# Kernel tuning notes

Hardware: AMD Instinct MI355X
Metric: run time of the kernel (lower is better)

Reference implementation:

```python
import jax, jax.numpy as jnp
import numpy as np

D_INPUT = 1024
N_HEADS = 16
D_INNER = 64
SEQ = 1024
PREV = 1024
BS = 4
LN_EPS = 1e-5


def _rel_shift(x):
    # x: (i, j, b, h) -> Transformer-XL relative shift trick
    i, j, b, h = x.shape
    zero_pad = jnp.zeros((i, 1, b, h), dtype=x.dtype)
    return jnp.concatenate([zero_pad, x], axis=1).reshape(j + 1, i, b, h)[1:].reshape(i, j, b, h)


def setup_inputs() -> dict:
    key = jax.random.key(0)
    ks = jax.random.split(key, 9)
    w = 0.02
    return {
        "input_": jax.random.normal(ks[0], (SEQ, BS, D_INPUT), jnp.float32),
        "pos_embs": jax.random.normal(ks[1], (SEQ + PREV, D_INPUT), jnp.float32),
        "memory": jax.random.normal(ks[2], (PREV, BS, D_INPUT), jnp.float32),
        "u": jax.random.normal(ks[3], (N_HEADS, D_INNER), jnp.float32) * w,
        "v": jax.random.normal(ks[4], (N_HEADS, D_INNER), jnp.float32) * w,
        "W_kv": jax.random.normal(ks[5], (D_INPUT, 2 * N_HEADS * D_INNER), jnp.float32) * w,
        "W_q": jax.random.normal(ks[6], (D_INPUT, N_HEADS * D_INNER), jnp.float32) * w,
        "W_p": jax.random.normal(ks[7], (D_INPUT, N_HEADS * D_INNER), jnp.float32) * w,
        "W_out": jax.random.normal(ks[8], (N_HEADS * D_INNER, D_INPUT), jnp.float32) * w,
        "ln_g": jnp.ones((D_INPUT,), jnp.float32),
        "ln_b": jnp.zeros((D_INPUT,), jnp.float32),
    }


def reference(input_, pos_embs, memory, u, v, W_kv, W_q, W_p, W_out, ln_g, ln_b):
    S, B, D = input_.shape
    P = memory.shape[0]
    T = S + P
    H, d = u.shape
    scale = 1.0 / (d ** 0.5)

    x_mem = jnp.concatenate([memory, input_], axis=0)          # (T, B, D)
    kv = x_mem @ W_kv                                          # (T, B, 2*H*d)
    k, val = jnp.split(kv, 2, axis=-1)
    k = k.reshape(T, B, H, d)
    val = val.reshape(T, B, H, d)
    q = (input_ @ W_q).reshape(S, B, H, d)                     # (S, B, H, d)

    content_attn = jnp.einsum('ibhd,jbhd->ijbh', q + u, k)     # (S, T, B, H)
    p = (pos_embs @ W_p).reshape(T, H, d)                      # (T, H, d)
    position_attn = jnp.einsum('ibhd,jhd->ijbh', q + v, p)     # (S, T, B, H)
    position_attn = _rel_shift(position_attn)

    attn = jax.nn.softmax((content_attn + position_attn) * scale, axis=1)
    awv = jnp.einsum('ijbh,jbhd->ibhd', attn, val).reshape(S, B, H * d)

    out = input_ + awv @ W_out                                 # residual
    mu = jnp.mean(out, axis=-1, keepdims=True)
    var = jnp.mean(jnp.square(out - mu), axis=-1, keepdims=True)
    return (out - mu) * jax.lax.rsqrt(var + LN_EPS) * ln_g + ln_b
```

## Files before the change

### kernel.cpp

```cpp
#include <hip/hip_runtime.h>
#include <cstdint>
#include <cstddef>

#define S_  1024
#define B_  4
#define T_  2048
#define H_  16

typedef short     short8 __attribute__((ext_vector_type(8)));
typedef float     f32x4  __attribute__((ext_vector_type(4)));
typedef unsigned short u16x8 __attribute__((ext_vector_type(8)));

__device__ __forceinline__ unsigned short f2b(float f){
  uint32_t x = __builtin_bit_cast(uint32_t, f);
  x = (x + 0x7fffu + ((x >> 16) & 1u)) >> 16;
  return (unsigned short)x;
}
__device__ __forceinline__ unsigned short f2bt(float f){
  return (unsigned short)(__builtin_bit_cast(uint32_t, f) >> 16);
}
__device__ __forceinline__ float b2f(unsigned short u){
  return __builtin_bit_cast(float, ((uint32_t)u) << 16);
}

__device__ __forceinline__ void gl_lds16(const unsigned short* g, unsigned short* l){
  __builtin_amdgcn_global_load_lds(
      (const __attribute__((address_space(1))) void*)g,
      (__attribute__((address_space(3))) void*)l,
      16, 0, 0);
}

__global__ __launch_bounds__(256) void cvt_cat(
    const float* __restrict__ a, const float* __restrict__ bsrc,
    int splitElems, int total, unsigned short* __restrict__ out)
{
  int i = (blockIdx.x * 256 + threadIdx.x) * 4;
  if (i >= total) return;
  const float* src = (i < splitElems) ? (a + i) : (bsrc + (i - splitElems));
  float4 x = *(const float4*)src;
  ushort4 o;
  o.x = f2b(x.x); o.y = f2b(x.y); o.z = f2b(x.z); o.w = f2b(x.w);
  *(ushort4*)(out + i) = o;
}

__global__ __launch_bounds__(256) void wtrans(
    const float* __restrict__ in, unsigned short* __restrict__ out, int R, int C)
{
  __shared__ float tile[32][33];
  const int R0 = blockIdx.y * 32, C0 = blockIdx.x * 32;
  const int t = threadIdx.x;
  const int r = t >> 3, c4 = (t & 7) * 4;
  float4 x = *(const float4*)(in + (size_t)(R0 + r) * C + C0 + c4);
  tile[r][c4+0] = x.x; tile[r][c4+1] = x.y; tile[r][c4+2] = x.z; tile[r][c4+3] = x.w;
  __syncthreads();
  ushort4 o;
  o.x = f2b(tile[c4+0][r]); o.y = f2b(tile[c4+1][r]);
  o.z = f2b(tile[c4+2][r]); o.w = f2b(tile[c4+3][r]);
  *(ushort4*)(out + (size_t)(C0 + r) * R + R0 + c4) = o;
}

__global__ __launch_bounds__(256) void vtrans(
    const unsigned short* __restrict__ kvb, unsigned short* __restrict__ vtg)
{
  __shared__ __align__(16) unsigned short tile[64][72];
  const int t = threadIdx.x;
  const int bh = blockIdx.y;
  const int b = bh >> 4, h = bh & 15;
  const int t0 = blockIdx.x * 64;
  #pragma unroll
  for (int l = 0; l < 2; ++l){
    int idx = t + l * 256;
    int row = idx >> 3, seg = (idx & 7) * 8;
    u16x8 x = *(const u16x8*)(kvb + ((size_t)(t0 + row) * 4 + b) * 2048 + 1024 + h * 64 + seg);
    *(u16x8*)&tile[row][seg] = x;
  }
  __syncthreads();
  #pragma unroll
  for (int l = 0; l < 2; ++l){
    int idx = t + l * 256;
    int d = idx >> 3, nseg = (idx & 7) * 8;
    u16x8 o;
    #pragma unroll
    for (int j = 0; j < 8; ++j) o[j] = tile[nseg + j][d];
    *(u16x8*)(vtg + ((size_t)bh * 64 + d) * 2048 + t0 + nseg) = o;
  }
}

#define AS_IDX(row,k) ((((row) >> 3) * 512) + (((k) >> 3) * 64) + (((row) & 7) * 8) + ((k) & 7))

__global__ __launch_bounds__(256) void gemm_multi(
    const unsigned short* __restrict__ xb,
    const unsigned short* __restrict__ posb,
    const unsigned short* __restrict__ WkvT,
    const unsigned short* __restrict__ WqT,
    const unsigned short* __restrict__ WpT,
    unsigned short* __restrict__ kvb,
    unsigned short* __restrict__ qbb,
    unsigned short* __restrict__ pbb)
{
  const unsigned short *A, *BT;
  unsigned short* C;
  int N, local;
  int bx = blockIdx.x;
  if (bx < 1024){       A = xb;                       BT = WkvT; C = kvb; N = 2048; local = bx;        }
  else if (bx < 1280){  A = xb + (size_t)4096 * 1024; BT = WqT;  C = qbb; N = 1024; local = bx - 1024; }
  else {                A = posb;                     BT = WpT;  C = pbb; N = 1024; local = bx - 1280; }
  const int nb = N >> 7;
  const int M0 = (local / nb) * 128, N0 = (local % nb) * 128;
  const int K = 1024;

  __shared__ __align__(16) unsigned short As[128 * 64];
  __shared__ __align__(16) unsigned short Bs[128 * 64];
  const int t = threadIdx.x;
  const int w = t >> 6, lane = t & 63, quad = lane >> 4, l16 = lane & 15;
  const int wm = (w >> 1) * 64, wn = (w & 1) * 64;
  const int lr = lane & 7, lcb = lane >> 3;

  f32x4 acc[4][4] = {};

  for (int k0 = 0; k0 < K; k0 += 64){
    __syncthreads();
    #pragma unroll
    for (int i = 0; i < 4; ++i){
      int blk = 4 * w + i;
      gl_lds16(A  + (size_t)(M0 + 8 * blk + lr) * K + k0 + lcb * 8, As + blk * 512);
      gl_lds16(BT + (size_t)(N0 + 8 * blk + lr) * K + k0 + lcb * 8, Bs + blk * 512);
    }
    __syncthreads();
    #pragma unroll
    for (int ks = 0; ks < 2; ++ks){
      short8 af[4], bf[4];
      #pragma unroll
      for (int rt = 0; rt < 4; ++rt)
        af[rt] = *(short8*)&As[AS_IDX(wm + rt * 16 + l16, ks * 32 + quad * 8)];
      #pragma unroll
      for (int ct = 0; ct < 4; ++ct)
        bf[ct] = *(short8*)&Bs[AS_IDX(wn + ct * 16 + l16, ks * 32 + quad * 8)];
      #pragma unroll
      for (int rt = 0; rt < 4; ++rt)
        #pragma unroll
        for (int ct = 0; ct < 4; ++ct)
          acc[rt][ct] = __builtin_amdgcn_mfma_f32_16x16x32_bf16(af[rt], bf[ct], acc[rt][ct], 0, 0, 0);
    }
  }

  #pragma unroll
  for (int rt = 0; rt < 4; ++rt)
    #pragma unroll
    for (int r = 0; r < 4; ++r){
      int row = M0 + wm + rt * 16 + quad * 4 + r;
      #pragma unroll
      for (int ct = 0; ct < 4; ++ct)
        C[(size_t)row * N + N0 + wn + ct * 16 + l16] = f2b(acc[rt][ct][r]);
    }
}

__global__ __launch_bounds__(256) void gemm_outk(
    const unsigned short* __restrict__ A,
    const unsigned short* __restrict__ BT,
    float* __restrict__ OutP)
{
  const int K = 1024, N = 1024;
  const int k0s = blockIdx.z * 512, k0e = k0s + 512;
  float* outF = OutP + (size_t)blockIdx.z * 4096 * 1024;

  __shared__ __align__(16) unsigned short As[128 * 64];
  __shared__ __align__(16) unsigned short Bs[128 * 64];
  const int t = threadIdx.x;
  const int M0 = blockIdx.y * 128, N0 = blockIdx.x * 128;
  const int w = t >> 6, lane = t & 63, quad = lane >> 4, l16 = lane & 15;
  const int wm = (w >> 1) * 64, wn = (w & 1) * 64;
  const int lr = lane & 7, lcb = lane >> 3;

  f32x4 acc[4][4] = {};

  for (int k0 = k0s; k0 < k0e; k0 += 64){
    __syncthreads();
    #pragma unroll
    for (int i = 0; i < 4; ++i){
      int blk = 4 * w + i;
      gl_lds16(A  + (size_t)(M0 + 8 * blk + lr) * K + k0 + lcb * 8, As + blk * 512);
      gl_lds16(BT + (size_t)(N0 + 8 * blk + lr) * K + k0 + lcb * 8, Bs + blk * 512);
    }
    __syncthreads();
    #pragma unroll
    for (int ks = 0; ks < 2; ++ks){
      short8 af[4], bf[4];
      #pragma unroll
      for (int rt = 0; rt < 4; ++rt)
        af[rt] = *(short8*)&As[AS_IDX(wm + rt * 16 + l16, ks * 32 + quad * 8)];
      #pragma unroll
      for (int ct = 0; ct < 4; ++ct)
        bf[ct] = *(short8*)&Bs[AS_IDX(wn + ct * 16 + l16, ks * 32 + quad * 8)];
      #pragma unroll
      for (int rt = 0; rt < 4; ++rt)
        #pragma unroll
        for (int ct = 0; ct < 4; ++ct)
          acc[rt][ct] = __builtin_amdgcn_mfma_f32_16x16x32_bf16(af[rt], bf[ct], acc[rt][ct], 0, 0, 0);
    }
  }

  #pragma unroll
  for (int rt = 0; rt < 4; ++rt)
    #pragma unroll
    for (int r = 0; r < 4; ++r){
      int row = M0 + wm + rt * 16 + quad * 4 + r;
      #pragma unroll
      for (int ct = 0; ct < 4; ++ct)
        outF[(size_t)row * N + N0 + wn + ct * 16 + l16] = acc[rt][ct][r];
    }
}

__global__ __launch_bounds__(256, 3) void attn_mfma(
    const unsigned short* __restrict__ qb,
    const unsigned short* __restrict__ kvb,
    const unsigned short* __restrict__ pbm,
    const unsigned short* __restrict__ vtg,
    const float* __restrict__ ub, const float* __restrict__ vb,
    unsigned short* __restrict__ opart,
    float* __restrict__ lpart)
{
  __shared__ __align__(16) unsigned short Kc[64 * 64];
  __shared__ __align__(16) unsigned short VT[64 * 64];
  __shared__ __align__(16) unsigned short Pw[128 * 64];
  __shared__ __align__(16) unsigned short Pb[64 * 72];
  __shared__ unsigned short Sc[64 * 65];

  const int t = threadIdx.x;
  const int i0 = blockIdx.x * 64;
  const int bh = blockIdx.y;
  const int jh = blockIdx.z;
  const int b = bh >> 4, h = bh & 15;
  const int w = t >> 6, lane = t & 63, quad = lane >> 4, l16 = lane & 15;
  const int colbase = h * 64 + quad * 8;
  const int ctLo = 3 - w;

  short8 qu[2], qv[2][2];
  #pragma unroll
  for (int cs = 0; cs < 2; ++cs){
    int gr = i0 + 16 * w + l16 + cs;
    #pragma unroll
    for (int ks = 0; ks < 2; ++ks){
      u16x8 q8 = *(const u16x8*)(qb + ((size_t)gr * 4 + b) * 1024 + colbase + ks * 32);
      #pragma unroll
      for (int j = 0; j < 8; ++j){
        float f = b2f(q8[j]);
        qv[cs][ks][j] = (short)f2b(f + vb[colbase + ks * 32 + j]);
        if (cs == 0) qu[ks][j] = (short)f2b(f + ub[colbase + ks * 32 + j]);
      }
    }
  }

  f32x4 oacc[4] = {};
  float lsum[4] = {0.f, 0.f, 0.f, 0.f};

  u16x8 pk[2], pv2[2], pp[4];

  auto loadRegs = [&](int jc){
    const int j0 = jc * 64;
    const int D = j0 - i0;
    #pragma unroll
    for (int l = 0; l < 2; ++l){
      int idx = t + l * 256;
      int row = idx >> 3, cb = idx & 7;
      pk[l]  = *(const u16x8*)(kvb + ((size_t)(j0 + row) * 4 + b) * 2048 + h * 64 + cb * 8);
      pv2[l] = *(const u16x8*)(vtg + ((size_t)bh * 64 + row) * 2048 + j0 + cb * 8);
    }
    #pragma unroll
    for (int l = 0; l < 4; ++l){
      int idx = t + l * 256;
      int row = idx >> 3, cb = idx & 7;
      int pr;
      if (D <= 960)          pr = D + 960 + row;
      else if (D == 1024)    pr = (row < 64) ? (1984 + row) : (row - 65);
      else                   pr = D - 1089 + row;
      u16x8 x;
      if (pr >= 0 && pr < T_){
        x = *(const u16x8*)(pbm + (size_t)pr * 1024 + h * 64 + cb * 8);
      } else {
        for (int j = 0; j < 8; ++j) x[j] = 0;
      }
      pp[l] = x;
    }
  };

  auto storeRegs = [&](){
    #pragma unroll
    for (int l = 0; l < 2; ++l){
      int idx = t + l * 256;
      int row = idx >> 3, cb = idx & 7;
      int sw = (cb ^ (row & 7)) * 8;
      *(u16x8*)&Kc[row * 64 + sw] = pk[l];
      *(u16x8*)&VT[row * 64 + sw] = pv2[l];
    }
    #pragma unroll
    for (int l = 0; l < 4; ++l){
      int idx = t + l * 256;
      int row = idx >> 3, cb = idx & 7;
      *(u16x8*)&Pw[row * 64 + ((cb ^ (row & 7)) * 8)] = pp[l];
    }
  };

  const int jcs = jh * 16, jce = jcs + 16;
  loadRegs(jcs);

  #pragma unroll 1
  for (int jc = jcs; jc < jce; ++jc){
    const int j0 = jc * 64;
    const int D = j0 - i0;

    __syncthreads();
    storeRegs();
    if (jc + 1 < jce) loadRegs(jc + 1);
    __syncthreads();

    #pragma unroll
    for (int ci = 0; ci < 5; ++ci){
      int ct = ctLo + ci;
      int cs = (D <= 960) ? 0 : ((D >= 1088) ? 1 : ((ct >= 4) ? 1 : 0));
      f32x4 racc = {};
      #pragma unroll
      for (int ks = 0; ks < 2; ++ks){
        int rr = ct * 16 + l16;
        short8 bf = *(short8*)&Pw[rr * 64 + (((ks * 4 + quad) ^ (rr & 7)) * 8)];
        racc = __builtin_amdgcn_mfma_f32_16x16x32_bf16(qv[cs][ks], bf, racc, 0, 0, 0);
      }
      int c = ct * 16 + l16;
      #pragma unroll
      for (int r = 0; r < 4; ++r){
        int gm = 16 * w + quad * 4 + r;
        int n = c + gm - 63;
        if ((unsigned)n < 64u) Sc[gm * 65 + n] = f2bt(racc[r]);
      }
    }

    f32x4 cacc[4] = {};
    #pragma unroll
    for (int ks = 0; ks < 2; ++ks){
      #pragma unroll
      for (int ct = 0; ct < 4; ++ct){
        int rr = ct * 16 + l16;
        short8 bf = *(short8*)&Kc[rr * 64 + (((ks * 4 + quad) ^ (rr & 7)) * 8)];
        cacc[ct] = __builtin_amdgcn_mfma_f32_16x16x32_bf16(qu[ks], bf, cacc[ct], 0, 0, 0);
      }
    }

    #pragma unroll
    for (int ct = 0; ct < 4; ++ct){
      #pragma unroll
      for (int r = 0; r < 4; ++r){
        int gm = 16 * w + quad * 4 + r;
        int n = ct * 16 + l16;
        float s = (cacc[ct][r] + b2f(Sc[gm * 65 + n])) * 0.125f;
        float e = __expf(s - 16.f);
        lsum[r] += e;
        Pb[gm * 72 + n] = f2bt(e);
      }
    }

    #pragma unroll
    for (int ks = 0; ks < 2; ++ks){
      short8 af = *(short8*)&Pb[(16 * w + l16) * 72 + ks * 32 + quad * 8];
      #pragma unroll
      for (int dt = 0; dt < 4; ++dt){
        int rr = dt * 16 + l16;
        short8 bf = *(short8*)&VT[rr * 64 + (((ks * 4 + quad) ^ (rr & 7)) * 8)];
        oacc[dt] = __builtin_amdgcn_mfma_f32_16x16x32_bf16(af, bf, oacc[dt], 0, 0, 0);
      }
    }
  }

  unsigned short* ob = opart + (size_t)jh * 4096 * 1024;
  float* lb = lpart + (size_t)jh * 4096 * 16;
  #pragma unroll
  for (int r = 0; r < 4; ++r){
    float red = lsum[r];
    #pragma unroll
    for (int mk = 1; mk < 16; mk <<= 1)
      red += __shfl_xor(red, mk, 64);
    int srow = i0 + 16 * w + quad * 4 + r;
    int grow = srow * 4 + b;
    #pragma unroll
    for (int dt = 0; dt < 4; ++dt)
      ob[(size_t)grow * 1024 + h * 64 + dt * 16 + l16] = f2bt(oacc[dt][r]);
    if (l16 == 0) lb[(size_t)grow * 16 + h] = red;
  }
}

__global__ __launch_bounds__(256) void attn_combine(
    const unsigned short* __restrict__ opart, const float* __restrict__ lpart,
    unsigned short* __restrict__ awvb)
{
  const int grow = blockIdx.x, t = threadIdx.x;
  const int d4 = t * 4, h = t >> 4;
  float l = lpart[(size_t)grow * 16 + h] + lpart[(size_t)4096 * 16 + grow * 16 + h];
  float inv = 1.f / l;
  ushort4 a = *(const ushort4*)(opart + (size_t)grow * 1024 + d4);
  ushort4 c = *(const ushort4*)(opart + (size_t)4096 * 1024 + grow * 1024 + d4);
  ushort4 o;
  o.x = f2bt((b2f(a.x) + b2f(c.x)) * inv);
  o.y = f2bt((b2f(a.y) + b2f(c.y)) * inv);
  o.z = f2bt((b2f(a.z) + b2f(c.z)) * inv);
  o.w = f2bt((b2f(a.w) + b2f(c.w)) * inv);
  *(ushort4*)(awvb + (size_t)grow * 1024 + d4) = o;
}

__global__ __launch_bounds__(256) void ln2_kernel(
    const float* __restrict__ inp, const float* __restrict__ OutP,
    const float* __restrict__ g, const float* __restrict__ bb,
    float* __restrict__ out)
{
  const int row = blockIdx.x, t = threadIdx.x;
  float4 x  = *(const float4*)(inp  + (size_t)row * 1024 + t * 4);
  float4 p0 = *(const float4*)(OutP + (size_t)row * 1024 + t * 4);
  float4 p1 = *(const float4*)(OutP + (size_t)4096 * 1024 + row * 1024 + t * 4);
  x.x += p0.x + p1.x; x.y += p0.y + p1.y; x.z += p0.z + p1.z; x.w += p0.w + p1.w;
  float s  = x.x + x.y + x.z + x.w;
  float s2 = x.x*x.x + x.y*x.y + x.z*x.z + x.w*x.w;
  #pragma unroll
  for (int o = 32; o > 0; o >>= 1){
    s  += __shfl_down(s, o);
    s2 += __shfl_down(s2, o);
  }
  __shared__ float rs[4], rs2[4];
  int w = t >> 6, lane = t & 63;
  if (lane == 0){ rs[w] = s; rs2[w] = s2; }
  __syncthreads();
  s  = rs[0] + rs[1] + rs[2] + rs[3];
  s2 = rs2[0] + rs2[1] + rs2[2] + rs2[3];
  float mu   = s * (1.f/1024.f);
  float var  = s2 * (1.f/1024.f) - mu*mu;
  float rstd = rsqrtf(var + 1e-5f);
  float4 gg = *(const float4*)(g + t*4);
  float4 bv = *(const float4*)(bb + t*4);
  float4 o;
  o.x = (x.x - mu)*rstd*gg.x + bv.x;
  o.y = (x.y - mu)*rstd*gg.y + bv.y;
  o.z = (x.z - mu)*rstd*gg.z + bv.z;
  o.w = (x.w - mu)*rstd*gg.w + bv.w;
  *(float4*)(out + (size_t)row * 1024 + t * 4) = o;
}

extern "C" void kernel_launch(void* const* d_in, const int* in_sizes, int n_in,
                              void* d_out, int out_size, void* d_ws, size_t ws_size,
                              hipStream_t stream) {
  (void)in_sizes; (void)n_in; (void)out_size; (void)ws_size;
  const float* input_ = (const float*)d_in[0];
  const float* pos    = (const float*)d_in[1];
  const float* mem    = (const float*)d_in[2];
  const float* u      = (const float*)d_in[3];
  const float* v      = (const float*)d_in[4];
  const float* Wkv    = (const float*)d_in[5];
  const float* Wq     = (const float*)d_in[6];
  const float* Wp     = (const float*)d_in[7];
  const float* Wout   = (const float*)d_in[8];
  const float* lng    = (const float*)d_in[9];
  const float* lnb    = (const float*)d_in[10];
  float* out = (float*)d_out;

  unsigned short* ws   = (unsigned short*)d_ws;
  unsigned short* xb    = ws;
  unsigned short* posb  = xb    + (size_t)8192*1024;
  unsigned short* WkvT  = posb  + (size_t)2048*1024;
  unsigned short* WqT   = WkvT  + (size_t)2048*1024;
  unsigned short* WpT   = WqT   + (size_t)1024*1024;
  unsigned short* WoutT = WpT   + (size_t)1024*1024;
  unsigned short* kvb   = WoutT + (size_t)1024*1024;
  unsigned short* qbb   = kvb   + (size_t)8192*2048;
  unsigned short* pbb   = qbb   + (size_t)4096*1024;
  unsigned short* vtg   = pbb   + (size_t)2048*1024;
  unsigned short* awvb  = vtg   + (size_t)4096*2048;

  unsigned short* opart = xb;
  float*          lpart = (float*)posb;
  float*          OutP  = (float*)kvb;

  cvt_cat<<<8192, 256, 0, stream>>>(mem, input_, 4096*1024, 8192*1024, xb);
  cvt_cat<<<2048, 256, 0, stream>>>(pos, pos, 2048*1024, 2048*1024, posb);
  wtrans<<<dim3(64, 32), 256, 0, stream>>>(Wkv,  WkvT, 1024, 2048);
  wtrans<<<dim3(32, 32), 256, 0, stream>>>(Wq,   WqT,  1024, 1024);
  wtrans<<<dim3(32, 32), 256, 0, stream>>>(Wp,   WpT,  1024, 1024);
  wtrans<<<dim3(32, 32), 256, 0, stream>>>(Wout, WoutT,1024, 1024);

  gemm_multi<<<1408, 256, 0, stream>>>(xb, posb, WkvT, WqT, WpT, kvb, qbb, pbb);

  vtrans<<<dim3(32, 64), 256, 0, stream>>>(kvb, vtg);

  attn_mfma<<<dim3(16, 64, 2), 256, 0, stream>>>(qbb, kvb, pbb, vtg, u, v, opart, lpart);
  attn_combine<<<4096, 256, 0, stream>>>(opart, lpart, awvb);

  gemm_outk<<<dim3(8, 32, 2), 256, 0, stream>>>(awvb, WoutT, OutP);
  ln2_kernel<<<4096, 256, 0, stream>>>(input_, OutP, lng, lnb, out);
}
```

Baseline: 406.7 us.

## Reuse half of positional tile, read V from global, merge score buffers

```diff
diff --git a/kernel.cpp b/kernel.cpp
--- a/kernel.cpp
+++ b/kernel.cpp
@@ -211,7 +211,9 @@
     }
 }
 
-__global__ __launch_bounds__(256, 3) void attn_mfma(
+#define SP_IX(gm,n) ((gm) * 64 + ((n) ^ (((gm) & 12) << 2)))
+
+__global__ __launch_bounds__(256, 4) void attn_mfma(
     const unsigned short* __restrict__ qb,
     const unsigned short* __restrict__ kvb,
     const unsigned short* __restrict__ pbm,
@@ -221,10 +223,8 @@
     float* __restrict__ lpart)
 {
   __shared__ __align__(16) unsigned short Kc[64 * 64];
-  __shared__ __align__(16) unsigned short VT[64 * 64];
   __shared__ __align__(16) unsigned short Pw[128 * 64];
-  __shared__ __align__(16) unsigned short Pb[64 * 72];
-  __shared__ unsigned short Sc[64 * 65];
+  __shared__ __align__(16) unsigned short SP[64 * 64];
 
   const int t = threadIdx.x;
   const int i0 = blockIdx.x * 64;
@@ -235,6 +235,9 @@
   const int colbase = h * 64 + quad * 8;
   const int ctLo = 3 - w;
 
+  const float SCQ = 0.1803368801f;
+  const float EOF_ = 23.0831206f;
+
   short8 qu[2], qv[2][2];
   #pragma unroll
   for (int cs = 0; cs < 2; ++cs){
@@ -245,8 +248,8 @@
       #pragma unroll
       for (int j = 0; j < 8; ++j){
         float f = b2f(q8[j]);
-        qv[cs][ks][j] = (short)f2b(f + vb[colbase + ks * 32 + j]);
-        if (cs == 0) qu[ks][j] = (short)f2b(f + ub[colbase + ks * 32 + j]);
+        qv[cs][ks][j] = (short)f2b((f + vb[colbase + ks * 32 + j]) * SCQ);
+        if (cs == 0) qu[ks][j] = (short)f2b((f + ub[colbase + ks * 32 + j]) * SCQ);
       }
     }
   }
@@ -254,18 +257,20 @@
   f32x4 oacc[4] = {};
   float lsum[4] = {0.f, 0.f, 0.f, 0.f};
 
-  u16x8 pk[2], pv2[2], pp[4];
-
-  auto loadRegs = [&](int jc){
+  u16x8 pk[2], pp[4];
+
+  auto loadKV = [&](int jc){
     const int j0 = jc * 64;
-    const int D = j0 - i0;
     #pragma unroll
     for (int l = 0; l < 2; ++l){
       int idx = t + l * 256;
       int row = idx >> 3, cb = idx & 7;
-      pk[l]  = *(const u16x8*)(kvb + ((size_t)(j0 + row) * 4 + b) * 2048 + h * 64 + cb * 8);
-      pv2[l] = *(const u16x8*)(vtg + ((size_t)bh * 64 + row) * 2048 + j0 + cb * 8);
-    }
+      pk[l] = *(const u16x8*)(kvb + ((size_t)(j0 + row) * 4 + b) * 2048 + h * 64 + cb * 8);
+    }
+  };
+
+  auto loadPPfull = [&](int jc){
+    const int D = jc * 64 - i0;
     #pragma unroll
     for (int l = 0; l < 4; ++l){
       int idx = t + l * 256;
@@ -284,15 +289,32 @@
     }
   };
 
-  auto storeRegs = [&](){
+  auto loadPPhalf = [&](int jc){
+    const int D = jc * 64 - i0;
+    #pragma unroll
+    for (int l = 0; l < 2; ++l){
+      int idx = t + l * 256;
+      int rowh = idx >> 3, cb = idx & 7;
+      int pr = (D <= 960) ? (D + 1024 + rowh) : (D - 1025 + rowh);
+      u16x8 x;
+      if (pr >= 0 && pr < T_){
+        x = *(const u16x8*)(pbm + (size_t)pr * 1024 + h * 64 + cb * 8);
+      } else {
+        for (int j = 0; j < 8; ++j) x[j] = 0;
+      }
+      pp[l] = x;
+    }
+  };
+
+  auto storeK = [&](){
     #pragma unroll
     for (int l = 0; l < 2; ++l){
       int idx = t + l * 256;
       int row = idx >> 3, cb = idx & 7;
-      int sw = (cb ^ (row & 7)) * 8;
-      *(u16x8*)&Kc[row * 64 + sw] = pk[l];
-      *(u16x8*)&VT[row * 64 + sw] = pv2[l];
-    }
+      *(u16x8*)&Kc[row * 64 + ((cb ^ (row & 7)) * 8)] = pk[l];
+    }
+  };
+  auto storePPfull = [&](){
     #pragma unroll
     for (int l = 0; l < 4; ++l){
       int idx = t + l * 256;
@@ -300,9 +322,19 @@
       *(u16x8*)&Pw[row * 64 + ((cb ^ (row & 7)) * 8)] = pp[l];
     }
   };
+  auto storePPhalf = [&](int physh){
+    #pragma unroll
+    for (int l = 0; l < 2; ++l){
+      int idx = t + l * 256;
+      int rowh = idx >> 3, cb = idx & 7;
+      *(u16x8*)&Pw[(physh * 64 + rowh) * 64 + ((cb ^ (rowh & 7)) * 8)] = pp[l];
+    }
+  };
 
   const int jcs = jh * 16, jce = jcs + 16;
-  loadRegs(jcs);
+  loadKV(jcs);
+  loadPPfull(jcs);
+  int par = 0;
 
   #pragma unroll 1
   for (int jc = jcs; jc < jce; ++jc){
@@ -310,9 +342,18 @@
     const int D = j0 - i0;
 
     __syncthreads();
-    storeRegs();
-    if (jc + 1 < jce) loadRegs(jc + 1);
+    storeK();
+    if (jc == jcs) storePPfull(); else storePPhalf(1 ^ par);
+    if (jc + 1 < jce){ loadKV(jc + 1); loadPPhalf(jc + 1); }
     __syncthreads();
+
+    const unsigned short* vg = vtg + ((size_t)bh * 64) * 2048 + j0;
+    u16x8 vf[8];
+    #pragma unroll
+    for (int ks = 0; ks < 2; ++ks)
+      #pragma unroll
+      for (int dt = 0; dt < 4; ++dt)
+        vf[ks * 4 + dt] = *(const u16x8*)(vg + (size_t)(dt * 16 + l16) * 2048 + ks * 32 + quad * 8);
 
     #pragma unroll
     for (int ci = 0; ci < 5; ++ci){
@@ -322,7 +363,8 @@
       #pragma unroll
       for (int ks = 0; ks < 2; ++ks){
         int rr = ct * 16 + l16;
-        short8 bf = *(short8*)&Pw[rr * 64 + (((ks * 4 + quad) ^ (rr & 7)) * 8)];
+        int prow = ((rr >> 6) ^ par) * 64 + (rr & 63);
+        short8 bf = *(short8*)&Pw[prow * 64 + (((ks * 4 + quad) ^ (rr & 7)) * 8)];
         racc = __builtin_amdgcn_mfma_f32_16x16x32_bf16(qv[cs][ks], bf, racc, 0, 0, 0);
       }
       int c = ct * 16 + l16;
@@ -330,7 +372,7 @@
       for (int r = 0; r < 4; ++r){
         int gm = 16 * w + quad * 4 + r;
         int n = c + gm - 63;
-        if ((unsigned)n < 64u) Sc[gm * 65 + n] = f2bt(racc[r]);
+        if ((unsigned)n < 64u) SP[SP_IX(gm, n)] = f2bt(racc[r]);
       }
     }
 
@@ -351,23 +393,24 @@
       for (int r = 0; r < 4; ++r){
         int gm = 16 * w + quad * 4 + r;
         int n = ct * 16 + l16;
-        float s = (cacc[ct][r] + b2f(Sc[gm * 65 + n])) * 0.125f;
-        float e = __expf(s - 16.f);
+        int ix = SP_IX(gm, n);
+        float s = cacc[ct][r] + b2f(SP[ix]);
+        float e = __builtin_amdgcn_exp2f(s - EOF_);
         lsum[r] += e;
-        Pb[gm * 72 + n] = f2bt(e);
+        SP[ix] = f2bt(e);
       }
     }
 
     #pragma unroll
     for (int ks = 0; ks < 2; ++ks){
-      short8 af = *(short8*)&Pb[(16 * w + l16) * 72 + ks * 32 + quad * 8];
-      #pragma unroll
-      for (int dt = 0; dt < 4; ++dt){
-        int rr = dt * 16 + l16;
-        short8 bf = *(short8*)&VT[rr * 64 + (((ks * 4 + quad) ^ (rr & 7)) * 8)];
-        oacc[dt] = __builtin_amdgcn_mfma_f32_16x16x32_bf16(af, bf, oacc[dt], 0, 0, 0);
-      }
-    }
+      short8 af = *(short8*)&SP[SP_IX(16 * w + l16, ks * 32 + quad * 8)];
+      #pragma unroll
+      for (int dt = 0; dt < 4; ++dt)
+        oacc[dt] = __builtin_amdgcn_mfma_f32_16x16x32_bf16(
+            af, (short8)vf[ks * 4 + dt], oacc[dt], 0, 0, 0);
+    }
+
+    par ^= 1;
   }
 
   unsigned short* ob = opart + (size_t)jh * 4096 * 1024;
```

After: 803.2 us. +97.5%, slower.
